# Optimization experiments

Hardware: AMD Instinct MI355X
Metric: run time of the kernel (lower is better)

## Reference

```python
import jax, jax.numpy as jnp
import numpy as np

NUM_GRAPHS = 64

def _sage(x_src, x_dst, ei, Wl, bl, Wr):
    # PyG SAGEConv (aggr='mean', root_weight=True): lin_l(mean_j x_j) + lin_r(x_dst)
    src, dst = ei[0], ei[1]
    n_dst = x_dst.shape[0]
    msg = jnp.take(x_src, src, axis=0)                      # [E, D] gather
    s = jax.ops.segment_sum(msg, dst, num_segments=n_dst)   # [N_dst, D] scatter-add
    deg = jax.ops.segment_sum(jnp.ones(src.shape, x_src.dtype), dst, num_segments=n_dst)
    mean = s / jnp.maximum(deg, 1.0)[:, None]
    return (mean @ Wl + bl) + x_dst @ Wr

def _mean_pool(x, batch):
    s = jax.ops.segment_sum(x, batch, num_segments=NUM_GRAPHS)
    c = jax.ops.segment_sum(jnp.ones((x.shape[0],), x.dtype), batch, num_segments=NUM_GRAPHS)
    return s / jnp.maximum(c, 1.0)[:, None]

def setup_inputs() -> dict:
    key = jax.random.key(0)
    ks = jax.random.split(key, 40)
    N, E, D, H, C = 50000, 1600000, 128, 128, 2
    inp = {}
    inp['x_user'] = jax.random.normal(ks[0], (N, D), jnp.float32)
    inp['x_drug'] = jax.random.normal(ks[1], (N, D), jnp.float32)
    inp['ei_ud'] = jax.random.randint(ks[2], (2, E), 0, N)
    inp['ei_du'] = jax.random.randint(ks[3], (2, E), 0, N)
    inp['ei_uu'] = jax.random.randint(ks[4], (2, E), 0, N)
    inp['batch_user'] = jnp.sort(jax.random.randint(ks[5], (N,), 0, NUM_GRAPHS))
    inp['batch_drug'] = jnp.sort(jax.random.randint(ks[6], (N,), 0, NUM_GRAPHS))
    i = 7
    for lyr in (1, 2):
        for et in ('ud', 'du', 'uu'):
            inp[f'Wl{lyr}_{et}'] = jax.random.normal(ks[i], (D, H), jnp.float32) / np.float32(np.sqrt(D)); i += 1
            inp[f'bl{lyr}_{et}'] = jnp.zeros((H,), jnp.float32)
            inp[f'Wr{lyr}_{et}'] = jax.random.normal(ks[i], (D, H), jnp.float32) / np.float32(np.sqrt(D)); i += 1
    inp['W1'] = jax.random.normal(ks[i], (2 * H, H), jnp.float32) / np.float32(np.sqrt(2 * H)); i += 1
    inp['b1'] = jnp.zeros((H,), jnp.float32)
    inp['W2'] = jax.random.normal(ks[i], (H, C), jnp.float32) / np.float32(np.sqrt(H)); i += 1
    inp['b2'] = jnp.zeros((C,), jnp.float32)
    return inp

def reference(x_user, x_drug, ei_ud, ei_du, ei_uu, batch_user, batch_drug,
              Wl1_ud, bl1_ud, Wr1_ud, Wl1_du, bl1_du, Wr1_du, Wl1_uu, bl1_uu, Wr1_uu,
              Wl2_ud, bl2_ud, Wr2_ud, Wl2_du, bl2_du, Wr2_du, Wl2_uu, bl2_uu, Wr2_uu,
              W1, b1, W2, b2):
    # Layer 1 (HeteroConv sums per-dst-type contributions), then ReLU
    u1 = _sage(x_drug, x_user, ei_du, Wl1_du, bl1_du, Wr1_du) \
       + _sage(x_user, x_user, ei_uu, Wl1_uu, bl1_uu, Wr1_uu)
    d1 = _sage(x_user, x_drug, ei_ud, Wl1_ud, bl1_ud, Wr1_ud)
    u1 = jax.nn.relu(u1)
    d1 = jax.nn.relu(d1)
    # Layer 2 (no ReLU in original before pooling)
    u2 = _sage(d1, u1, ei_du, Wl2_du, bl2_du, Wr2_du) \
       + _sage(u1, u1, ei_uu, Wl2_uu, bl2_uu, Wr2_uu)
    d2 = _sage(u1, d1, ei_ud, Wl2_ud, bl2_ud, Wr2_ud)
    # Per-node-type global mean pool, concat along feature dim
    x_pool = jnp.concatenate([_mean_pool(u2, batch_user), _mean_pool(d2, batch_drug)], axis=1)
    h = jax.nn.relu(x_pool @ W1 + b1)
    logits = h @ W2 + b2
    return jax.nn.log_softmax(logits, axis=1)
```

## Files before the change

### kernel.cpp

```cpp
#include <hip/hip_runtime.h>

#define NG 64
#define REP 8
#define GSC 512
#define NBK_MAX 1024

typedef __bf16 bf16x8 __attribute__((ext_vector_type(8)));
typedef float  f32x4  __attribute__((ext_vector_type(4)));

__device__ __forceinline__ ushort f2bf(float f) {
    unsigned int b = __float_as_uint(f);
    b += 0x7fffu + ((b >> 16) & 1u);
    return (ushort)(b >> 16);
}

__global__ __launch_bounds__(256) void bucket_count3(
    const int* __restrict__ d0, int E0, int nbk0, int* __restrict__ c0,
    const int* __restrict__ d1, int E1, int nbk1, int* __restrict__ c1,
    const int* __restrict__ d2, int E2, int nbk2, int* __restrict__ c2)
{
    const int* dst; int E, nbk; int* cntA;
    if (blockIdx.y == 0) { dst = d0; E = E0; nbk = nbk0; cntA = c0; }
    else if (blockIdx.y == 1) { dst = d1; E = E1; nbk = nbk1; cntA = c1; }
    else { dst = d2; E = E2; nbk = nbk2; cntA = c2; }
    __shared__ int h[NBK_MAX];
    for (int i = threadIdx.x; i < nbk; i += 256) h[i] = 0;
    __syncthreads();
    int chunk = (E + GSC - 1) / GSC;
    int i0 = blockIdx.x * chunk, i1 = min(E, i0 + chunk);
    for (int i = i0 + threadIdx.x; i < i1; i += 256)
        atomicAdd(&h[dst[i] >> 6], 1);
    __syncthreads();
    for (int i = threadIdx.x; i < nbk; i += 256)
        cntA[(size_t)i * GSC + blockIdx.x] = h[i];
}

__global__ __launch_bounds__(GSC) void scan_blocks3(
    int* __restrict__ c0, int nbk0, int* __restrict__ bt0,
    int* __restrict__ c1, int nbk1, int* __restrict__ bt1,
    int* __restrict__ c2, int nbk2, int* __restrict__ bt2)
{
    int* cntA; int nbk; int* btot;
    if (blockIdx.y == 0) { cntA = c0; nbk = nbk0; btot = bt0; }
    else if (blockIdx.y == 1) { cntA = c1; nbk = nbk1; btot = bt1; }
    else { cntA = c2; nbk = nbk2; btot = bt2; }
    int b = blockIdx.x;
    if (b >= nbk) return;
    int t = threadIdx.x, lane = t & 63, wv = t >> 6;
    __shared__ int wsum[8];
    int v = cntA[(size_t)b * GSC + t];
    int x = v;
    #pragma unroll
    for (int off = 1; off < 64; off <<= 1) { int u = __shfl_up(x, off, 64); if (lane >= off) x += u; }
    if (lane == 63) wsum[wv] = x;
    __syncthreads();
    if (wv == 0 && lane < 8) {
        int w = wsum[lane];
        #pragma unroll
        for (int off = 1; off < 8; off <<= 1) { int u = __shfl_up(w, off, 64); if (lane >= off) w += u; }
        wsum[lane] = w;
    }
    __syncthreads();
    int incl = x + (wv > 0 ? wsum[wv - 1] : 0);
    cntA[(size_t)b * GSC + t] = incl - v;
    if (t == GSC - 1) btot[b] = incl;
}

__global__ __launch_bounds__(1024) void scan_buckets3(
    const int* __restrict__ bt0, int nbk0, int* __restrict__ bb0,
    const int* __restrict__ bt1, int nbk1, int* __restrict__ bb1,
    const int* __restrict__ bt2, int nbk2, int* __restrict__ bb2)
{
    const int* btot; int nbk; int* bbase;
    if (blockIdx.x == 0) { btot = bt0; nbk = nbk0; bbase = bb0; }
    else if (blockIdx.x == 1) { btot = bt1; nbk = nbk1; bbase = bb1; }
    else { btot = bt2; nbk = nbk2; bbase = bb2; }
    int t = threadIdx.x, lane = t & 63, wv = t >> 6;
    __shared__ int wsum[16];
    int v = (t < nbk) ? btot[t] : 0;
    int x = v;
    #pragma unroll
    for (int off = 1; off < 64; off <<= 1) { int u = __shfl_up(x, off, 64); if (lane >= off) x += u; }
    if (lane == 63) wsum[wv] = x;
    __syncthreads();
    if (wv == 0 && lane < 16) {
        int w = wsum[lane];
        #pragma unroll
        for (int off = 1; off < 16; off <<= 1) { int u = __shfl_up(w, off, 64); if (lane >= off) w += u; }
        wsum[lane] = w;
    }
    __syncthreads();
    int incl = x + (wv > 0 ? wsum[wv - 1] : 0);
    if (t <= nbk) bbase[t] = incl - v;
}

__global__ __launch_bounds__(256) void bucket_scatter3(
    const int* __restrict__ s0, const int* __restrict__ d0, int E0, int nbk0,
    const int* __restrict__ ba0, const int* __restrict__ bb0, int2* __restrict__ eb0,
    const int* __restrict__ s1, const int* __restrict__ d1, int E1, int nbk1,
    const int* __restrict__ ba1, const int* __restrict__ bb1, int2* __restrict__ eb1,
    const int* __restrict__ s2, const int* __restrict__ d2, int E2, int nbk2,
    const int* __restrict__ ba2, const int* __restrict__ bb2, int2* __restrict__ eb2)
{
    const int *src, *dst, *basesA, *bbase; int E, nbk; int2* ebuf;
    if (blockIdx.y == 0) { src = s0; dst = d0; E = E0; nbk = nbk0; basesA = ba0; bbase = bb0; ebuf = eb0; }
    else if (blockIdx.y == 1) { src = s1; dst = d1; E = E1; nbk = nbk1; basesA = ba1; bbase = bb1; ebuf = eb1; }
    else { src = s2; dst = d2; E = E2; nbk = nbk2; basesA = ba2; bbase = bb2; ebuf = eb2; }
    __shared__ int cur[NBK_MAX];
    for (int i = threadIdx.x; i < nbk; i += 256)
        cur[i] = bbase[i] + basesA[(size_t)i * GSC + blockIdx.x];
    __syncthreads();
    int chunk = (E + GSC - 1) / GSC;
    int i0 = blockIdx.x * chunk, i1 = min(E, i0 + chunk);
    for (int i = i0 + threadIdx.x; i < i1; i += 256) {
        int d = dst[i];
        int pos = atomicAdd(&cur[d >> 6], 1);
        ebuf[pos] = make_int2(src[i], d);
    }
}

__global__ __launch_bounds__(256) void csrify3(
    const int2* __restrict__ eb0, const int* __restrict__ bb0, int M0, int E0, int nbk0,
    int* __restrict__ rp0, int* __restrict__ cs0,
    const int2* __restrict__ eb1, const int* __restrict__ bb1, int M1, int E1, int nbk1,
    int* __restrict__ rp1, int* __restrict__ cs1,
    const int2* __restrict__ eb2, const int* __restrict__ bb2, int M2, int E2, int nbk2,
    int* __restrict__ rp2, int* __restrict__ cs2)
{
    const int2* ebuf; const int* bbase; int M, E, nbk; int *rp, *csr;
    if (blockIdx.y == 0) { ebuf = eb0; bbase = bb0; M = M0; E = E0; nbk = nbk0; rp = rp0; csr = cs0; }
    else if (blockIdx.y == 1) { ebuf = eb1; bbase = bb1; M = M1; E = E1; nbk = nbk1; rp = rp1; csr = cs1; }
    else { ebuf = eb2; bbase = bb2; M = M2; E = E2; nbk = nbk2; rp = rp2; csr = cs2; }
    if ((int)blockIdx.x >= nbk) return;
    __shared__ int hist[64], cur[64];
    int t = threadIdx.x;
    if (t < 64) hist[t] = 0;
    __syncthreads();
    int e0 = bbase[blockIdx.x], e1 = bbase[blockIdx.x + 1];
    for (int e = e0 + t; e < e1; e += 256)
        atomicAdd(&hist[ebuf[e].y & 63], 1);
    __syncthreads();
    if (t < 64) {
        int x = hist[t];
        #pragma unroll
        for (int off = 1; off < 64; off <<= 1) { int u = __shfl_up(x, off, 64); if (t >= off) x += u; }
        int ex = x - hist[t];
        cur[t] = ex;
        int row = (blockIdx.x << 6) + t;
        if (row < M) rp[row] = e0 + ex;
    }
    if (blockIdx.x == 0 && t == 0) rp[M] = E;
    __syncthreads();
    for (int e = e0 + t; e < e1; e += 256) {
        int2 p = ebuf[e];
        int pos = atomicAdd(&cur[p.y & 63], 1);
        csr[e0 + pos] = p.x;
    }
}

__global__ void add2_kernel(const float* __restrict__ a, const float* __restrict__ b,
                            float* __restrict__ o, int n) {
    int i = blockIdx.x * blockDim.x + threadIdx.x;
    if (i < n) o[i] = a[i] + b[i];
}

__global__ void cvt_kernel(const float* __restrict__ x, ushort* __restrict__ o, int n4) {
    int i = blockIdx.x * blockDim.x + threadIdx.x;
    if (i >= n4) return;
    float4 v = ((const float4*)x)[i];
    ushort4 r;
    r.x = f2bf(v.x); r.y = f2bf(v.y); r.z = f2bf(v.z); r.w = f2bf(v.w);
    ((ushort4*)o)[i] = r;
}

__global__ void wprep_kernel(
    const float* __restrict__ Wa0, const float* __restrict__ Wb0, ushort* __restrict__ Wt0,
    const float* __restrict__ Wa1, ushort* __restrict__ Wt1,
    const float* __restrict__ Wa2, ushort* __restrict__ Wt2,
    const float* __restrict__ Wa3, ushort* __restrict__ Wt3,
    const float* __restrict__ Wa4, ushort* __restrict__ Wt4)
{
    const float* Wa; const float* Wb = nullptr; ushort* Wt;
    switch (blockIdx.x) {
        case 0: Wa = Wa0; Wb = Wb0; Wt = Wt0; break;
        case 1: Wa = Wa1; Wt = Wt1; break;
        case 2: Wa = Wa2; Wt = Wt2; break;
        case 3: Wa = Wa3; Wt = Wt3; break;
        default: Wa = Wa4; Wt = Wt4; break;
    }
    for (int idx = threadIdx.x; idx < 128 * 128; idx += 256) {
        int n = idx >> 7, k = idx & 127;
        float v = Wa[k * 128 + n];
        if (Wb) v += Wb[k * 128 + n];
        Wt[idx] = f2bf(v);
    }
}

__global__ void bounds_kernel(const int* __restrict__ bu, int nu,
                              const int* __restrict__ bd, int nd,
                              int* __restrict__ bndu, int* __restrict__ bndd)
{
    const int* b = blockIdx.x == 0 ? bu : bd;
    int        n = blockIdx.x == 0 ? nu : nd;
    int*       o = blockIdx.x == 0 ? bndu : bndd;
    int g = threadIdx.x;
    if (g > NG) return;
    int lo = 0, hi = n;
    while (lo < hi) { int m = (lo + hi) >> 1; if (b[m] < g) lo = m + 1; else hi = m; }
    o[g] = lo;
}

#define GATHER16(J)                                                                  \
    {                                                                                \
        unsigned int v[16];                                                          \
        _Pragma("unroll")                                                            \
        for (int k = 0; k < 16; ++k)                                                 \
            v[k] = *(const unsigned int*)&xb[(size_t)csr[(J) + k] * 128 + lane * 2]; \
        _Pragma("unroll")                                                            \
        for (int k = 0; k < 16; ++k) {                                               \
            sx += __uint_as_float(v[k] << 16);                                       \
            sy += __uint_as_float(v[k] & 0xffff0000u);                               \
        }                                                                            \
    }

__global__ __launch_bounds__(256) void agg3_kernel(
    const ushort* __restrict__ x0, const int* __restrict__ rpa, const int* __restrict__ csa, int Ma, ushort* __restrict__ ma,
    const ushort* __restrict__ x1, const int* __restrict__ rpb, const int* __restrict__ csb, int Mb, ushort* __restrict__ mb,
    const ushort* __restrict__ x2, const int* __restrict__ rpc, const int* __restrict__ csc, int Mc, ushort* __restrict__ mc)
{
    const ushort* xb; const int *rp, *csr; int M; ushort* mean;
    if (blockIdx.y == 0) { xb = x0; rp = rpa; csr = csa; M = Ma; mean = ma; }
    else if (blockIdx.y == 1) { xb = x1; rp = rpb; csr = csb; M = Mb; mean = mb; }
    else { xb = x2; rp = rpc; csr = csc; M = Mc; mean = mc; }
    int wave = threadIdx.x >> 6, lane = threadIdx.x & 63;
    int row = blockIdx.x * 4 + wave;
    if (row >= M) return;
    int s0 = rp[row], s1 = rp[row + 1];
    float sx = 0.f, sy = 0.f;
    int j = s0;
    for (; j + 16 <= s1; j += 16) GATHER16(j)
    for (; j < s1; ++j) {
        unsigned int v = *(const unsigned int*)&xb[(size_t)csr[j] * 128 + lane * 2];
        sx += __uint_as_float(v << 16);
        sy += __uint_as_float(v & 0xffff0000u);
    }
    int deg = s1 - s0;
    float sc = 1.f / (float)(deg > 1 ? deg : 1);
    unsigned int pk = (unsigned int)f2bf(sx * sc) | ((unsigned int)f2bf(sy * sc) << 16);
    *(unsigned int*)&mean[(size_t)row * 128 + lane * 2] = pk;
}

template<int NA>
__global__ __launch_bounds__(256) void gemm_mfma(
    const ushort* __restrict__ A0, const ushort* __restrict__ A1, const ushort* __restrict__ A2,
    const ushort* __restrict__ Wt0, const ushort* __restrict__ Wt1, const ushort* __restrict__ Wt2,
    int M, const float* __restrict__ bias, ushort* __restrict__ C)
{
    int wave = threadIdx.x >> 6, lane = threadIdx.x & 63;
    int row0 = blockIdx.x * 64 + wave * 16;
    int r  = lane & 15;
    int kg = lane >> 4;
    f32x4 acc[8];
    #pragma unroll
    for (int nt = 0; nt < 8; ++nt) acc[nt] = (f32x4){0.f, 0.f, 0.f, 0.f};

    int arow = row0 + r;
    int arow_c = arow < M ? arow : 0;
    #pragma unroll
    for (int term = 0; term < NA; ++term) {
        const ushort* A  = (term == 0) ? A0  : (term == 1 ? A1  : A2);
        const ushort* Wt = (term == 0) ? Wt0 : (term == 1 ? Wt1 : Wt2);
        #pragma unroll
        for (int kk = 0; kk < 4; ++kk) {
            bf16x8 a = *(const bf16x8*)&A[(size_t)arow_c * 128 + kk * 32 + kg * 8];
            #pragma unroll
            for (int nt = 0; nt < 8; ++nt) {
                bf16x8 b = *(const bf16x8*)&Wt[(size_t)(nt * 16 + r) * 128 + kk * 32 + kg * 8];
                acc[nt] = __builtin_amdgcn_mfma_f32_16x16x32_bf16(a, b, acc[nt], 0, 0, 0);
            }
        }
    }

    #pragma unroll
    for (int nt = 0; nt < 8; ++nt) {
        int col = nt * 16 + r;
        float bv = bias[col];
        #pragma unroll
        for (int j = 0; j < 4; ++j) {
            int orow = row0 + kg * 4 + j;
            if (orow < M) {
                float v = fmaxf(acc[nt][j] + bv, 0.f);
                C[(size_t)orow * 128 + col] = f2bf(v);
            }
        }
    }
}

__global__ __launch_bounds__(256) void aggpool3_kernel(
    const ushort* __restrict__ x0, const int* __restrict__ rpa, const int* __restrict__ csa,
    const int* __restrict__ ba, int Ma, float* __restrict__ pa,
    const ushort* __restrict__ x1, const int* __restrict__ rpb, const int* __restrict__ csb,
    const int* __restrict__ bb, int Mb, float* __restrict__ pb,
    const ushort* __restrict__ x2, const int* __restrict__ rpc, const int* __restrict__ csc,
    const int* __restrict__ bc, int Mc, float* __restrict__ pc)
{
    const ushort* xb; const int *rp, *csr, *batch; int M; float* pool;
    if (blockIdx.y == 0) { xb = x0; rp = rpa; csr = csa; batch = ba; M = Ma; pool = pa; }
    else if (blockIdx.y == 1) { xb = x1; rp = rpb; csr = csb; batch = bb; M = Mb; pool = pb; }
    else { xb = x2; rp = rpc; csr = csc; batch = bc; M = Mc; pool = pc; }
    int wave = threadIdx.x >> 6, lane = threadIdx.x & 63;
    int r0 = (blockIdx.x * 4 + wave) * 4;
    if (r0 >= M) return;
    int r1 = min(M, r0 + 4);
    float* p = pool + (size_t)(blockIdx.x & (REP - 1)) * NG * 128;
    float ax = 0.f, ay = 0.f;
    int curg = batch[r0];
    for (int row = r0; row < r1; ++row) {
        int g = batch[row];
        if (g != curg) {
            atomicAdd(&p[curg * 128 + lane * 2],     ax);
            atomicAdd(&p[curg * 128 + lane * 2 + 1], ay);
            ax = 0.f; ay = 0.f; curg = g;
        }
        int s0 = rp[row], s1 = rp[row + 1];
        float sx = 0.f, sy = 0.f;
        int j = s0;
        for (; j + 16 <= s1; j += 16) GATHER16(j)
        for (; j < s1; ++j) {
            unsigned int v = *(const unsigned int*)&xb[(size_t)csr[j] * 128 + lane * 2];
            sx += __uint_as_float(v << 16);
            sy += __uint_as_float(v & 0xffff0000u);
        }
        int deg = s1 - s0;
        float sc = 1.f / (float)(deg > 1 ? deg : 1);
        ax += sx * sc; ay += sy * sc;
    }
    atomicAdd(&p[curg * 128 + lane * 2],     ax);
    atomicAdd(&p[curg * 128 + lane * 2 + 1], ay);
}

__global__ __launch_bounds__(256) void pool2_kernel(
    const ushort* __restrict__ u1b, const ushort* __restrict__ d1b,
    const int* __restrict__ bndu, const int* __restrict__ bndd,
    float* __restrict__ pu1, float* __restrict__ pd1)
{
    const ushort* xb; const int* bnd; float* pool;
    if (blockIdx.y == 0) { xb = u1b; bnd = bndu; pool = pu1; }
    else { xb = d1b; bnd = bndd; pool = pd1; }
    int g = blockIdx.x;
    int lo = bnd[g], hi = bnd[g + 1];
    int c2 = threadIdx.x & 63, half = threadIdx.x >> 6;
    float sx = 0.f, sy = 0.f;
    for (int r = lo + half; r < hi; r += 4) {
        unsigned int v = *(const unsigned int*)&xb[(size_t)r * 128 + c2 * 2];
        sx += __uint_as_float(v << 16);
        sy += __uint_as_float(v & 0xffff0000u);
    }
    __shared__ float ls[256 * 2];
    ls[threadIdx.x * 2]     = sx;
    ls[threadIdx.x * 2 + 1] = sy;
    __syncthreads();
    if (half == 0) {
        float ox = ls[c2 * 2] + ls[(64 + c2) * 2] + ls[(128 + c2) * 2] + ls[(192 + c2) * 2];
        float oy = ls[c2 * 2 + 1] + ls[(64 + c2) * 2 + 1] + ls[(128 + c2) * 2 + 1] + ls[(192 + c2) * 2 + 1];
        pool[g * 128 + c2 * 2]     = ox;
        pool[g * 128 + c2 * 2 + 1] = oy;
    }
}

__global__ __launch_bounds__(128) void final_kernel(
    const float* __restrict__ pmdu, const float* __restrict__ pmuu, const float* __restrict__ pmud,
    const float* __restrict__ pu1,  const float* __restrict__ pd1,
    const int* __restrict__ bndu, const int* __restrict__ bndd,
    const float* __restrict__ Wl2_du, const float* __restrict__ bl2_du, const float* __restrict__ Wr2_du,
    const float* __restrict__ Wl2_uu, const float* __restrict__ bl2_uu, const float* __restrict__ Wr2_uu,
    const float* __restrict__ Wl2_ud, const float* __restrict__ bl2_ud, const float* __restrict__ Wr2_ud,
    const float* __restrict__ W1, const float* __restrict__ b1,
    const float* __restrict__ W2, const float* __restrict__ b2,
    float* __restrict__ out)
{
    int g = blockIdx.x, t = threadIdx.x;
    __shared__ float smdu[128], smuu[128], smud[128], su1[128], sd1[128];
    __shared__ float xrow[256], h[128], lg[2];
    float vdu = 0.f, vuu = 0.f, vud = 0.f;
    #pragma unroll
    for (int r = 0; r < REP; ++r) {
        vdu += pmdu[(size_t)r * NG * 128 + g * 128 + t];
        vuu += pmuu[(size_t)r * NG * 128 + g * 128 + t];
        vud += pmud[(size_t)r * NG * 128 + g * 128 + t];
    }
    smdu[t] = vdu;
    smuu[t] = vuu;
    smud[t] = vud;
    su1[t]  = pu1[g * 128 + t];
    sd1[t]  = pd1[g * 128 + t];
    __syncthreads();
    float ncu = (float)(bndu[g + 1] - bndu[g]);
    float ncd = (float)(bndd[g + 1] - bndd[g]);
    float cu = ncu > 1.f ? ncu : 1.f, cd = ncd > 1.f ? ncd : 1.f;
    float accu = ncu * (bl2_du[t] + bl2_uu[t]);
    float accd = ncd * bl2_ud[t];
    for (int k = 0; k < 128; ++k) {
        accu += smdu[k] * Wl2_du[k * 128 + t]
              + smuu[k] * Wl2_uu[k * 128 + t]
              + su1[k]  * (Wr2_du[k * 128 + t] + Wr2_uu[k * 128 + t]);
        accd += smud[k] * Wl2_ud[k * 128 + t]
              + sd1[k]  * Wr2_ud[k * 128 + t];
    }
    xrow[t]       = accu / cu;
    xrow[128 + t] = accd / cd;
    __syncthreads();
    float hh = b1[t];
    for (int k = 0; k < 256; ++k) hh += xrow[k] * W1[k * 128 + t];
    h[t] = fmaxf(hh, 0.f);
    __syncthreads();
    if (t < 2) {
        float l = b2[t];
        for (int k = 0; k < 128; ++k) l += h[k] * W2[k * 2 + t];
        lg[t] = l;
    }
    __syncthreads();
    if (t == 0) {
        float m = fmaxf(lg[0], lg[1]);
        float lse = m + logf(expf(lg[0] - m) + expf(lg[1] - m));
        out[g * 2 + 0] = lg[0] - lse;
        out[g * 2 + 1] = lg[1] - lse;
    }
}

extern "C" void kernel_launch(void* const* d_in, const int* in_sizes, int n_in,
                              void* d_out, int out_size, void* d_ws, size_t ws_size,
                              hipStream_t stream)
{
    const float* x_user = (const float*)d_in[0];
    const float* x_drug = (const float*)d_in[1];
    const int* ei_ud = (const int*)d_in[2];
    const int* ei_du = (const int*)d_in[3];
    const int* ei_uu = (const int*)d_in[4];
    const int* batch_u = (const int*)d_in[5];
    const int* batch_d = (const int*)d_in[6];
    const float* Wl1_ud = (const float*)d_in[7];  const float* bl1_ud = (const float*)d_in[8];  const float* Wr1_ud = (const float*)d_in[9];
    const float* Wl1_du = (const float*)d_in[10]; const float* bl1_du = (const float*)d_in[11]; const float* Wr1_du = (const float*)d_in[12];
    const float* Wl1_uu = (const float*)d_in[13]; const float* bl1_uu = (const float*)d_in[14]; const float* Wr1_uu = (const float*)d_in[15];
    const float* Wl2_ud = (const float*)d_in[16]; const float* bl2_ud = (const float*)d_in[17]; const float* Wr2_ud = (const float*)d_in[18];
    const float* Wl2_du = (const float*)d_in[19]; const float* bl2_du = (const float*)d_in[20]; const float* Wr2_du = (const float*)d_in[21];
    const float* Wl2_uu = (const float*)d_in[22]; const float* bl2_uu = (const float*)d_in[23]; const float* Wr2_uu = (const float*)d_in[24];
    const float* W1 = (const float*)d_in[25]; const float* b1 = (const float*)d_in[26];
    const float* W2 = (const float*)d_in[27]; const float* b2 = (const float*)d_in[28];
    (void)n_in; (void)out_size; (void)ws_size;

    const int Nu = in_sizes[0] / 128;
    const int Nd = in_sizes[1] / 128;
    const int E_ud = in_sizes[2] / 2;
    const int E_du = in_sizes[3] / 2;
    const int E_uu = in_sizes[4] / 2;
    const int nbk_u = (Nu + 63) >> 6;
    const int nbk_d = (Nd + 63) >> 6;
    const int nbk_max = nbk_u > nbk_d ? nbk_u : nbk_d;
    const int Nmax = Nu > Nd ? Nu : Nd;

    char* ws = (char*)d_ws;
    size_t off = 0;
    auto alloc = [&](size_t bytes) -> void* {
        void* p = ws + off;
        off = (off + bytes + 255) & ~(size_t)255;
        return p;
    };
    int2* ebuf_ud = (int2*)alloc((size_t)E_ud * 8);
    int2* ebuf_du = (int2*)alloc((size_t)E_du * 8);
    int2* ebuf_uu = (int2*)alloc((size_t)E_uu * 8);
    int* cntA_ud = (int*)alloc((size_t)NBK_MAX * GSC * 4);
    int* cntA_du = (int*)alloc((size_t)NBK_MAX * GSC * 4);
    int* cntA_uu = (int*)alloc((size_t)NBK_MAX * GSC * 4);
    int* btot_ud = (int*)alloc((size_t)NBK_MAX * 4);
    int* btot_du = (int*)alloc((size_t)NBK_MAX * 4);
    int* btot_uu = (int*)alloc((size_t)NBK_MAX * 4);
    int* bbase_ud = (int*)alloc((size_t)(NBK_MAX + 1) * 4);
    int* bbase_du = (int*)alloc((size_t)(NBK_MAX + 1) * 4);
    int* bbase_uu = (int*)alloc((size_t)(NBK_MAX + 1) * 4);
    int* csr_ud = (int*)alloc((size_t)E_ud * 4);
    int* csr_du = (int*)alloc((size_t)E_du * 4);
    int* csr_uu = (int*)alloc((size_t)E_uu * 4);
    int* rp_ud = (int*)alloc((size_t)(Nd + 1) * 4);
    int* rp_du = (int*)alloc((size_t)(Nu + 1) * 4);
    int* rp_uu = (int*)alloc((size_t)(Nu + 1) * 4);
    ushort* xb_u = (ushort*)alloc((size_t)Nu * 128 * 2);
    ushort* xb_d = (ushort*)alloc((size_t)Nd * 128 * 2);
    ushort* mean_du = (ushort*)ebuf_du;
    ushort* mean_uu = (ushort*)ebuf_uu;
    ushort* mean_ud = (ushort*)ebuf_ud;
    ushort* u1b = (ushort*)alloc((size_t)Nu * 128 * 2);
    ushort* d1b = (ushort*)alloc((size_t)Nd * 128 * 2);
    float* pmdu = (float*)alloc((size_t)REP * NG * 128 * 4);
    float* pmuu = (float*)alloc((size_t)REP * NG * 128 * 4);
    float* pmud = (float*)alloc((size_t)REP * NG * 128 * 4);
    char* zero2_beg = (char*)pmdu;
    char* zero2_end = ws + off;
    float* pu1  = (float*)alloc(NG * 128 * 4);
    float* pd1  = (float*)alloc(NG * 128 * 4);
    int* bnd_u = (int*)alloc((NG + 1) * 4);
    int* bnd_d = (int*)alloc((NG + 1) * 4);
    ushort* Wt_ru  = (ushort*)alloc(128 * 128 * 2);
    ushort* Wt_ldu = (ushort*)alloc(128 * 128 * 2);
    ushort* Wt_luu = (ushort*)alloc(128 * 128 * 2);
    ushort* Wt_rud = (ushort*)alloc(128 * 128 * 2);
    ushort* Wt_lud = (ushort*)alloc(128 * 128 * 2);
    float* b1s_u  = (float*)alloc(128 * 4);

    const int* dst_ud = ei_ud + E_ud;
    const int* dst_du = ei_du + E_du;
    const int* dst_uu = ei_uu + E_uu;

    bucket_count3<<<dim3(GSC, 3), 256, 0, stream>>>(
        dst_ud, E_ud, nbk_d, cntA_ud,
        dst_du, E_du, nbk_u, cntA_du,
        dst_uu, E_uu, nbk_u, cntA_uu);
    scan_blocks3<<<dim3(nbk_max, 3), GSC, 0, stream>>>(
        cntA_ud, nbk_d, btot_ud,
        cntA_du, nbk_u, btot_du,
        cntA_uu, nbk_u, btot_uu);
    scan_buckets3<<<3, 1024, 0, stream>>>(
        btot_ud, nbk_d, bbase_ud,
        btot_du, nbk_u, bbase_du,
        btot_uu, nbk_u, bbase_uu);
    bucket_scatter3<<<dim3(GSC, 3), 256, 0, stream>>>(
        ei_ud, dst_ud, E_ud, nbk_d, cntA_ud, bbase_ud, ebuf_ud,
        ei_du, dst_du, E_du, nbk_u, cntA_du, bbase_du, ebuf_du,
        ei_uu, dst_uu, E_uu, nbk_u, cntA_uu, bbase_uu, ebuf_uu);
    csrify3<<<dim3(nbk_max, 3), 256, 0, stream>>>(
        ebuf_ud, bbase_ud, Nd, E_ud, nbk_d, rp_ud, csr_ud,
        ebuf_du, bbase_du, Nu, E_du, nbk_u, rp_du, csr_du,
        ebuf_uu, bbase_uu, Nu, E_uu, nbk_u, rp_uu, csr_uu);

    bounds_kernel<<<2, NG + 1, 0, stream>>>(batch_u, Nu, batch_d, Nd, bnd_u, bnd_d);
    cvt_kernel<<<(Nu * 32 + 255) / 256, 256, 0, stream>>>(x_user, xb_u, Nu * 32);
    cvt_kernel<<<(Nd * 32 + 255) / 256, 256, 0, stream>>>(x_drug, xb_d, Nd * 32);
    wprep_kernel<<<5, 256, 0, stream>>>(Wr1_du, Wr1_uu, Wt_ru,
                                        Wl1_du, Wt_ldu, Wl1_uu, Wt_luu,
                                        Wr1_ud, Wt_rud, Wl1_ud, Wt_lud);
    add2_kernel<<<1, 128, 0, stream>>>(bl1_du, bl1_uu, b1s_u, 128);
    hipMemsetAsync(zero2_beg, 0, (size_t)(zero2_end - zero2_beg), stream);

    agg3_kernel<<<dim3((Nmax + 3) / 4, 3), 256, 0, stream>>>(
        xb_d, rp_du, csr_du, Nu, mean_du,
        xb_u, rp_uu, csr_uu, Nu, mean_uu,
        xb_u, rp_ud, csr_ud, Nd, mean_ud);

    gemm_mfma<3><<<(Nu + 63) / 64, 256, 0, stream>>>(xb_u, mean_du, mean_uu,
                                                     Wt_ru, Wt_ldu, Wt_luu, Nu, b1s_u, u1b);
    gemm_mfma<2><<<(Nd + 63) / 64, 256, 0, stream>>>(xb_d, mean_ud, nullptr,
                                                     Wt_rud, Wt_lud, nullptr, Nd, bl1_ud, d1b);

    aggpool3_kernel<<<dim3((Nmax + 15) / 16, 3), 256, 0, stream>>>(
        d1b, rp_du, csr_du, batch_u, Nu, pmdu,
        u1b, rp_uu, csr_uu, batch_u, Nu, pmuu,
        u1b, rp_ud, csr_ud, batch_d, Nd, pmud);

    pool2_kernel<<<dim3(NG, 2), 256, 0, stream>>>(u1b, d1b, bnd_u, bnd_d, pu1, pd1);

    final_kernel<<<NG, 128, 0, stream>>>(pmdu, pmuu, pmud, pu1, pd1, bnd_u, bnd_d,
                                         Wl2_du, bl2_du, Wr2_du,
                                         Wl2_uu, bl2_uu, Wr2_uu,
                                         Wl2_ud, bl2_ud, Wr2_ud,
                                         W1, b1, W2, b2, (float*)d_out);
}
```

Baseline: 671.9 us.

## Store gathered node features and layer-1 outputs as FP8 to halve gather traffic

Adds a software FP8 (e4m3-like) encoder and decoder. The input features are now also converted to FP8, and the layer-1 GEMM writes its ReLU outputs in FP8, so the irregular neighbor gathers in agg3, aggpool3 and pool2 read one byte per element instead of two. The aim is to cut memory traffic in the gather-bound aggregation kernels. In exchange it costs extra ALU work per element for decoding, an extra FP8 write in the conversion kernel, and a large precision loss that could break accuracy tolerances.

Measured after the change: 654.7 us. 2.6% less time.

```diff
diff --git a/kernel.cpp b/kernel.cpp
--- a/kernel.cpp
+++ b/kernel.cpp
@@ -12,6 +12,20 @@
     unsigned int b = __float_as_uint(f);
     b += 0x7fffu + ((b >> 16) & 1u);
     return (ushort)(b >> 16);
+}
+
+__device__ __forceinline__ float fp8_to_f32(unsigned v8) {
+    unsigned b = ((v8 & 0x80u) << 24) | ((v8 & 0x7fu) << 20);
+    return __uint_as_float(b) * 1.329227995784916e36f;
+}
+__device__ __forceinline__ unsigned char f2fp8(float f) {
+    float a = fabsf(f);
+    unsigned s = (__float_as_uint(f) >> 24) & 0x80u;
+    if (a < 0.015625f) return (unsigned char)0;
+    if (a > 440.f) return (unsigned char)(s | 0x7eu);
+    unsigned b = __float_as_uint(a * 7.52316384526264e-37f);
+    b += 0x7ffffu + ((b >> 20) & 1u);
+    return (unsigned char)(s | ((b >> 20) & 0x7fu));
 }
 
 __global__ __launch_bounds__(256) void bucket_count3(
@@ -164,13 +178,17 @@
     if (i < n) o[i] = a[i] + b[i];
 }
 
-__global__ void cvt_kernel(const float* __restrict__ x, ushort* __restrict__ o, int n4) {
+__global__ void cvt_dual_kernel(const float* __restrict__ x, ushort* __restrict__ ob,
+                                unsigned char* __restrict__ o8, int n4) {
     int i = blockIdx.x * blockDim.x + threadIdx.x;
     if (i >= n4) return;
     float4 v = ((const float4*)x)[i];
-    ushort4 r;
-    r.x = f2bf(v.x); r.y = f2bf(v.y); r.z = f2bf(v.z); r.w = f2bf(v.w);
-    ((ushort4*)o)[i] = r;
+    ushort4 rb;
+    rb.x = f2bf(v.x); rb.y = f2bf(v.y); rb.z = f2bf(v.z); rb.w = f2bf(v.w);
+    ((ushort4*)ob)[i] = rb;
+    uchar4 r8;
+    r8.x = f2fp8(v.x); r8.y = f2fp8(v.y); r8.z = f2fp8(v.z); r8.w = f2fp8(v.w);
+    ((uchar4*)o8)[i] = r8;
 }
 
 __global__ void wprep_kernel(
@@ -210,39 +228,46 @@
     o[g] = lo;
 }
 
-#define GATHER16(J)                                                                  \
+#define GATHER8(J)                                                                   \
     {                                                                                \
-        unsigned int v[16];                                                          \
-        _Pragma("unroll")                                                            \
-        for (int k = 0; k < 16; ++k)                                                 \
-            v[k] = *(const unsigned int*)&xb[(size_t)csr[(J) + k] * 128 + lane * 2]; \
-        _Pragma("unroll")                                                            \
-        for (int k = 0; k < 16; ++k) {                                               \
-            sx += __uint_as_float(v[k] << 16);                                       \
-            sy += __uint_as_float(v[k] & 0xffff0000u);                               \
-        }                                                                            \
+        ushort w0 = *(const ushort*)&xf8[(size_t)csr[(J) + 0] * 128 + lane * 2];     \
+        ushort w1 = *(const ushort*)&xf8[(size_t)csr[(J) + 1] * 128 + lane * 2];     \
+        ushort w2 = *(const ushort*)&xf8[(size_t)csr[(J) + 2] * 128 + lane * 2];     \
+        ushort w3 = *(const ushort*)&xf8[(size_t)csr[(J) + 3] * 128 + lane * 2];     \
+        ushort w4 = *(const ushort*)&xf8[(size_t)csr[(J) + 4] * 128 + lane * 2];     \
+        ushort w5 = *(const ushort*)&xf8[(size_t)csr[(J) + 5] * 128 + lane * 2];     \
+        ushort w6 = *(const ushort*)&xf8[(size_t)csr[(J) + 6] * 128 + lane * 2];     \
+        ushort w7 = *(const ushort*)&xf8[(size_t)csr[(J) + 7] * 128 + lane * 2];     \
+        sx += fp8_to_f32(w0 & 0xffu) + fp8_to_f32(w1 & 0xffu)                        \
+            + fp8_to_f32(w2 & 0xffu) + fp8_to_f32(w3 & 0xffu)                        \
+            + fp8_to_f32(w4 & 0xffu) + fp8_to_f32(w5 & 0xffu)                        \
+            + fp8_to_f32(w6 & 0xffu) + fp8_to_f32(w7 & 0xffu);                       \
+        sy += fp8_to_f32(w0 >> 8) + fp8_to_f32(w1 >> 8)                              \
+            + fp8_to_f32(w2 >> 8) + fp8_to_f32(w3 >> 8)                              \
+            + fp8_to_f32(w4 >> 8) + fp8_to_f32(w5 >> 8)                              \
+            + fp8_to_f32(w6 >> 8) + fp8_to_f32(w7 >> 8);                             \
     }
 
 __global__ __launch_bounds__(256) void agg3_kernel(
-    const ushort* __restrict__ x0, const int* __restrict__ rpa, const int* __restrict__ csa, int Ma, ushort* __restrict__ ma,
-    const ushort* __restrict__ x1, const int* __restrict__ rpb, const int* __restrict__ csb, int Mb, ushort* __restrict__ mb,
-    const ushort* __restrict__ x2, const int* __restrict__ rpc, const int* __restrict__ csc, int Mc, ushort* __restrict__ mc)
-{
-    const ushort* xb; const int *rp, *csr; int M; ushort* mean;
-    if (blockIdx.y == 0) { xb = x0; rp = rpa; csr = csa; M = Ma; mean = ma; }
-    else if (blockIdx.y == 1) { xb = x1; rp = rpb; csr = csb; M = Mb; mean = mb; }
-    else { xb = x2; rp = rpc; csr = csc; M = Mc; mean = mc; }
+    const unsigned char* __restrict__ x0, const int* __restrict__ rpa, const int* __restrict__ csa, int Ma, ushort* __restrict__ ma,
+    const unsigned char* __restrict__ x1, const int* __restrict__ rpb, const int* __restrict__ csb, int Mb, ushort* __restrict__ mb,
+    const unsigned char* __restrict__ x2, const int* __restrict__ rpc, const int* __restrict__ csc, int Mc, ushort* __restrict__ mc)
+{
+    const unsigned char* xf8; const int *rp, *csr; int M; ushort* mean;
+    if (blockIdx.y == 0) { xf8 = x0; rp = rpa; csr = csa; M = Ma; mean = ma; }
+    else if (blockIdx.y == 1) { xf8 = x1; rp = rpb; csr = csb; M = Mb; mean = mb; }
+    else { xf8 = x2; rp = rpc; csr = csc; M = Mc; mean = mc; }
     int wave = threadIdx.x >> 6, lane = threadIdx.x & 63;
     int row = blockIdx.x * 4 + wave;
     if (row >= M) return;
     int s0 = rp[row], s1 = rp[row + 1];
     float sx = 0.f, sy = 0.f;
     int j = s0;
-    for (; j + 16 <= s1; j += 16) GATHER16(j)
+    for (; j + 8 <= s1; j += 8) GATHER8(j)
     for (; j < s1; ++j) {
-        unsigned int v = *(const unsigned int*)&xb[(size_t)csr[j] * 128 + lane * 2];
-        sx += __uint_as_float(v << 16);
-        sy += __uint_as_float(v & 0xffff0000u);
+        ushort w = *(const ushort*)&xf8[(size_t)csr[j] * 128 + lane * 2];
+        sx += fp8_to_f32(w & 0xffu);
+        sy += fp8_to_f32(w >> 8);
     }
     int deg = s1 - s0;
     float sc = 1.f / (float)(deg > 1 ? deg : 1);
@@ -254,7 +279,7 @@
 __global__ __launch_bounds__(256) void gemm_mfma(
     const ushort* __restrict__ A0, const ushort* __restrict__ A1, const ushort* __restrict__ A2,
     const ushort* __restrict__ Wt0, const ushort* __restrict__ Wt1, const ushort* __restrict__ Wt2,
-    int M, const float* __restrict__ bias, ushort* __restrict__ C)
+    int M, const float* __restrict__ bias, unsigned char* __restrict__ C)
 {
     int wave = threadIdx.x >> 6, lane = threadIdx.x & 63;
     int row0 = blockIdx.x * 64 + wave * 16;
@@ -290,24 +315,24 @@
             int orow = row0 + kg * 4 + j;
             if (orow < M) {
                 float v = fmaxf(acc[nt][j] + bv, 0.f);
-                C[(size_t)orow * 128 + col] = f2bf(v);
+                C[(size_t)orow * 128 + col] = f2fp8(v);
             }
         }
     }
 }
 
 __global__ __launch_bounds__(256) void aggpool3_kernel(
-    const ushort* __restrict__ x0, const int* __restrict__ rpa, const int* __restrict__ csa,
+    const unsigned char* __restrict__ x0, const int* __restrict__ rpa, const int* __restrict__ csa,
     const int* __restrict__ ba, int Ma, float* __restrict__ pa,
-    const ushort* __restrict__ x1, const int* __restrict__ rpb, const int* __restrict__ csb,
+    const unsigned char* __restrict__ x1, const int* __restrict__ rpb, const int* __restrict__ csb,
     const int* __restrict__ bb, int Mb, float* __restrict__ pb,
-    const ushort* __restrict__ x2, const int* __restrict__ rpc, const int* __restrict__ csc,
+    const unsigned char* __restrict__ x2, const int* __restrict__ rpc, const int* __restrict__ csc,
     const int* __restrict__ bc, int Mc, float* __restrict__ pc)
 {
-    const ushort* xb; const int *rp, *csr, *batch; int M; float* pool;
-    if (blockIdx.y == 0) { xb = x0; rp = rpa; csr = csa; batch = ba; M = Ma; pool = pa; }
-    else if (blockIdx.y == 1) { xb = x1; rp = rpb; csr = csb; batch = bb; M = Mb; pool = pb; }
-    else { xb = x2; rp = rpc; csr = csc; batch = bc; M = Mc; pool = pc; }
+    const unsigned char* xf8; const int *rp, *csr, *batch; int M; float* pool;
+    if (blockIdx.y == 0) { xf8 = x0; rp = rpa; csr = csa; batch = ba; M = Ma; pool = pa; }
+    else if (blockIdx.y == 1) { xf8 = x1; rp = rpb; csr = csb; batch = bb; M = Mb; pool = pb; }
+    else { xf8 = x2; rp = rpc; csr = csc; batch = bc; M = Mc; pool = pc; }
     int wave = threadIdx.x >> 6, lane = threadIdx.x & 63;
     int r0 = (blockIdx.x * 4 + wave) * 4;
     if (r0 >= M) return;
@@ -325,11 +350,11 @@
         int s0 = rp[row], s1 = rp[row + 1];
         float sx = 0.f, sy = 0.f;
         int j = s0;
-        for (; j + 16 <= s1; j += 16) GATHER16(j)
+        for (; j + 8 <= s1; j += 8) GATHER8(j)
         for (; j < s1; ++j) {
-            unsigned int v = *(const unsigned int*)&xb[(size_t)csr[j] * 128 + lane * 2];
-            sx += __uint_as_float(v << 16);
-            sy += __uint_as_float(v & 0xffff0000u);
+            ushort w = *(const ushort*)&xf8[(size_t)csr[j] * 128 + lane * 2];
+            sx += fp8_to_f32(w & 0xffu);
+            sy += fp8_to_f32(w >> 8);
         }
         int deg = s1 - s0;
         float sc = 1.f / (float)(deg > 1 ? deg : 1);
@@ -340,21 +365,21 @@
 }
 
 __global__ __launch_bounds__(256) void pool2_kernel(
-    const ushort* __restrict__ u1b, const ushort* __restrict__ d1b,
+    const unsigned char* __restrict__ u1f, const unsigned char* __restrict__ d1f,
     const int* __restrict__ bndu, const int* __restrict__ bndd,
     float* __restrict__ pu1, float* __restrict__ pd1)
 {
-    const ushort* xb; const int* bnd; float* pool;
-    if (blockIdx.y == 0) { xb = u1b; bnd = bndu; pool = pu1; }
-    else { xb = d1b; bnd = bndd; pool = pd1; }
+    const unsigned char* xf8; const int* bnd; float* pool;
+    if (blockIdx.y == 0) { xf8 = u1f; bnd = bndu; pool = pu1; }
+    else { xf8 = d1f; bnd = bndd; pool = pd1; }
     int g = blockIdx.x;
     int lo = bnd[g], hi = bnd[g + 1];
     int c2 = threadIdx.x & 63, half = threadIdx.x >> 6;
     float sx = 0.f, sy = 0.f;
     for (int r = lo + half; r < hi; r += 4) {
-        unsigned int v = *(const unsigned int*)&xb[(size_t)r * 128 + c2 * 2];
-        sx += __uint_as_float(v << 16);
-        sy += __uint_as_float(v & 0xffff0000u);
+        ushort w = *(const ushort*)&xf8[(size_t)r * 128 + c2 * 2];
+        sx += fp8_to_f32(w & 0xffu);
+        sy += fp8_to_f32(w >> 8);
     }
     __shared__ float ls[256 * 2];
     ls[threadIdx.x * 2]     = sx;
@@ -486,11 +511,13 @@
     int* rp_uu = (int*)alloc((size_t)(Nu + 1) * 4);
     ushort* xb_u = (ushort*)alloc((size_t)Nu * 128 * 2);
     ushort* xb_d = (ushort*)alloc((size_t)Nd * 128 * 2);
+    unsigned char* xf8_u = (unsigned char*)alloc((size_t)Nu * 128);
+    unsigned char* xf8_d = (unsigned char*)alloc((size_t)Nd * 128);
     ushort* mean_du = (ushort*)ebuf_du;
     ushort* mean_uu = (ushort*)ebuf_uu;
     ushort* mean_ud = (ushort*)ebuf_ud;
-    ushort* u1b = (ushort*)alloc((size_t)Nu * 128 * 2);
-    ushort* d1b = (ushort*)alloc((size_t)Nd * 128 * 2);
+    unsigned char* u1f = (unsigned char*)alloc((size_t)Nu * 128);
+    unsigned char* d1f = (unsigned char*)alloc((size_t)Nd * 128);
     float* pmdu = (float*)alloc((size_t)REP * NG * 128 * 4);
     float* pmuu = (float*)alloc((size_t)REP * NG * 128 * 4);
     float* pmud = (float*)alloc((size_t)REP * NG * 128 * 4);
@@ -533,8 +560,8 @@
         ebuf_uu, bbase_uu, Nu, E_uu, nbk_u, rp_uu, csr_uu);
 
     bounds_kernel<<<2, NG + 1, 0, stream>>>(batch_u, Nu, batch_d, Nd, bnd_u, bnd_d);
-    cvt_kernel<<<(Nu * 32 + 255) / 256, 256, 0, stream>>>(x_user, xb_u, Nu * 32);
-    cvt_kernel<<<(Nd * 32 + 255) / 256, 256, 0, stream>>>(x_drug, xb_d, Nd * 32);
+    cvt_dual_kernel<<<(Nu * 32 + 255) / 256, 256, 0, stream>>>(x_user, xb_u, xf8_u, Nu * 32);
+    cvt_dual_kernel<<<(Nd * 32 + 255) / 256, 256, 0, stream>>>(x_drug, xb_d, xf8_d, Nd * 32);
     wprep_kernel<<<5, 256, 0, stream>>>(Wr1_du, Wr1_uu, Wt_ru,
                                         Wl1_du, Wt_ldu, Wl1_uu, Wt_luu,
                                         Wr1_ud, Wt_rud, Wl1_ud, Wt_lud);
@@ -542,21 +569,21 @@
     hipMemsetAsync(zero2_beg, 0, (size_t)(zero2_end - zero2_beg), stream);
 
     agg3_kernel<<<dim3((Nmax + 3) / 4, 3), 256, 0, stream>>>(
-        xb_d, rp_du, csr_du, Nu, mean_du,
-        xb_u, rp_uu, csr_uu, Nu, mean_uu,
-        xb_u, rp_ud, csr_ud, Nd, mean_ud);
+        xf8_d, rp_du, csr_du, Nu, mean_du,
+        xf8_u, rp_uu, csr_uu, Nu, mean_uu,
+        xf8_u, rp_ud, csr_ud, Nd, mean_ud);
 
     gemm_mfma<3><<<(Nu + 63) / 64, 256, 0, stream>>>(xb_u, mean_du, mean_uu,
-                                                     Wt_ru, Wt_ldu, Wt_luu, Nu, b1s_u, u1b);
+                                                     Wt_ru, Wt_ldu, Wt_luu, Nu, b1s_u, u1f);
     gemm_mfma<2><<<(Nd + 63) / 64, 256, 0, stream>>>(xb_d, mean_ud, nullptr,
-                                                     Wt_rud, Wt_lud, nullptr, Nd, bl1_ud, d1b);
+                                                     Wt_rud, Wt_lud, nullptr, Nd, bl1_ud, d1f);
 
     aggpool3_kernel<<<dim3((Nmax + 15) / 16, 3), 256, 0, stream>>>(
-        d1b, rp_du, csr_du, batch_u, Nu, pmdu,
-        u1b, rp_uu, csr_uu, batch_u, Nu, pmuu,
-        u1b, rp_ud, csr_ud, batch_d, Nd, pmud);
-
-    pool2_kernel<<<dim3(NG, 2), 256, 0, stream>>>(u1b, d1b, bnd_u, bnd_d, pu1, pd1);
+        d1f, rp_du, csr_du, batch_u, Nu, pmdu,
+        u1f, rp_uu, csr_uu, batch_u, Nu, pmuu,
+        u1f, rp_ud, csr_ud, batch_d, Nd, pmud);
+
+    pool2_kernel<<<dim3(NG, 2), 256, 0, stream>>>(u1f, d1f, bnd_u, bnd_d, pu1, pd1);
 
     final_kernel<<<NG, 128, 0, stream>>>(pmdu, pmuu, pmud, pu1, pd1, bnd_u, bnd_d,
                                          Wl2_du, bl2_du, Wr2_du,
```
